# Kernel tuning notes

Hardware: AMD Instinct MI355X
Metric: run time of the kernel (lower is better)

## Reference

```python
import jax, jax.numpy as jnp
import numpy as np

NUM_HEADS = 4

def setup_inputs() -> dict:
    key = jax.random.key(0)
    ks = jax.random.split(key, 5)
    B, T, F, C = 2, 128, 256, 256
    # weights scaled ~1/sqrt(C) so softmax is not saturated
    s = 1.0 / np.sqrt(C)
    return {
        "x": jax.random.normal(ks[0], (B, T, F, C), jnp.float32),
        "w_in": jax.random.normal(ks[1], (3 * C, C), jnp.float32) * s,
        "b_in": jax.random.normal(ks[2], (3 * C,), jnp.float32) * 0.01,
        "w_out": jax.random.normal(ks[3], (C, C), jnp.float32) * s,
        "b_out": jax.random.normal(ks[4], (C,), jnp.float32) * 0.01,
        "band": 16,
    }

def reference(x, w_in, b_in, w_out, b_out, band):
    B, T, F, C = x.shape
    H = NUM_HEADS
    D = C // H
    x2 = x.reshape(B * T, F, C)  # attention over frequency, independent per (B,T)
    qkv = x2 @ w_in.T + b_in  # [BT, F, 3C]
    q, k, v = jnp.split(qkv, 3, axis=-1)
    def heads(t):
        return t.reshape(B * T, F, H, D).transpose(0, 2, 1, 3)  # [BT, H, F, D]
    q, k, v = heads(q), heads(k), heads(v)
    scores = jnp.einsum('bhid,bhjd->bhij', q, k) / jnp.sqrt(jnp.asarray(D, x.dtype))
    i = jnp.arange(F)[:, None]
    j = jnp.arange(F)[None, :]
    keep = jnp.abs(i - j) <= band  # banded locality mask [F, F]
    scores = jnp.where(keep, scores, -jnp.inf)
    attn = jax.nn.softmax(scores, axis=-1)
    out = jnp.einsum('bhij,bhjd->bhid', attn, v)  # [BT, H, F, D]
    out = out.transpose(0, 2, 1, 3).reshape(B * T, F, C)
    y = out @ w_out.T + b_out
    return y.reshape(B, T, F, C)
```

## Files before the change

### kernel.cpp

```cpp
#include <hip/hip_runtime.h>
#include <hip/hip_bf16.h>
#include <cstdint>

typedef unsigned int u32;
typedef __attribute__((ext_vector_type(8))) __bf16 bf16x8;
typedef __attribute__((ext_vector_type(4))) float f32x4;
typedef __attribute__((ext_vector_type(4))) _Float16 half4;
typedef __attribute__((ext_vector_type(2))) __fp16 fp16x2;

#define BT_N 256
#define F_N 256
#define C_N 256
#define H_N 4
#define D_N 64
#define TC_N 768
#define M_N (BT_N * F_N)
#define VT_ST 268

__device__ __forceinline__ ushort f2bf(float f) {
  u32 u = __float_as_uint(f);
  u32 r = (u + 0x7fffu + ((u >> 16) & 1u)) >> 16;
  return (ushort)r;
}

__device__ __forceinline__ u32 pkbf(float a, float b) {
  return (u32)f2bf(a) | ((u32)f2bf(b) << 16);
}

__device__ __forceinline__ void gload_lds16(const ushort* g, ushort* l) {
  __builtin_amdgcn_global_load_lds(
      (const __attribute__((address_space(1))) u32*)g,
      (__attribute__((address_space(3))) u32*)l, 16, 0, 0);
}

__global__ __launch_bounds__(256) void cvt3_f32_bf16_k(
    const float* __restrict__ sx, ushort* __restrict__ dx, int nx4,
    const float* __restrict__ si, ushort* __restrict__ di, int ni4,
    const float* __restrict__ so, ushort* __restrict__ dq, int no4) {
  int idx = blockIdx.x * 256 + threadIdx.x;
  int stride = gridDim.x * 256;
  int ntot = nx4 + ni4 + no4;
  for (int i = idx; i < ntot; i += stride) {
    const float4* s;
    ushort* d;
    if (i < nx4) { s = (const float4*)sx + i; d = dx + (size_t)i * 4; }
    else if (i < nx4 + ni4) { int k = i - nx4; s = (const float4*)si + k; d = di + (size_t)k * 4; }
    else { int k = i - nx4 - ni4; s = (const float4*)so + k; d = dq + (size_t)k * 4; }
    float4 v = *s;
    *(uint2*)d = make_uint2(pkbf(v.x, v.y), pkbf(v.z, v.w));
  }
}

__global__ __launch_bounds__(256, 4) void gemm_qkv_sb(
    const ushort* __restrict__ Ap, const ushort* __restrict__ Bp,
    const float* __restrict__ bias, _Float16* __restrict__ Cp,
    int NTN, int nwg8) {
  __shared__ ushort smemH[128 * 64 * 2];

  const int tid = threadIdx.x;
  const int lane = tid & 63;
  const int wid = tid >> 6;
  const int wr = wid >> 1, wc = wid & 1;
  const int l15 = lane & 15, l4 = lane >> 4;
  const int b = blockIdx.x;
  const int bid = (b & 7) * nwg8 + (b >> 3);
  const int tm = bid / NTN;
  const int tn = bid - tm * NTN;
  const int rowBase = tm * 128, colBase = tn * 128;

  f32x4 acc[4][4] = {};

  const int ar = (tid >> 3);
  const int c8 = tid & 7;
  const int akk = ((c8 ^ (ar & 7)) << 3);
  const ushort* gB = Bp + (size_t)(colBase + ar) * 256 + akk;
  const ushort* gAh = Ap + (size_t)(rowBase + ar) * 256 + akk;

#pragma unroll
  for (int t = 0; t < 4; ++t) {
    const int k0 = t * 64;
#pragma unroll
    for (int c = 0; c < 4; ++c) {
      gload_lds16(gAh + (size_t)(c * 32) * 256 + k0,
                  smemH + (size_t)(c * 256 + (wid << 6)) * 8);
      gload_lds16(gB + (size_t)(c * 32) * 256 + k0,
                  smemH + 8192 + (size_t)(c * 256 + (wid << 6)) * 8);
    }
    __syncthreads();
    const ushort* As_ = smemH;
    const ushort* Bs_ = smemH + 8192;
#pragma unroll
    for (int kk = 0; kk < 2; ++kk) {
      bf16x8 af[4];
      bf16x8 bfr[4];
#pragma unroll
      for (int i2 = 0; i2 < 4; ++i2) {
        int row = wr * 64 + i2 * 16 + l15;
        af[i2] = *(const bf16x8*)(As_ + row * 64 + (((kk * 4 + l4) ^ (l15 & 7)) * 8));
      }
#pragma unroll
      for (int j2 = 0; j2 < 4; ++j2) {
        int row = wc * 64 + j2 * 16 + l15;
        bfr[j2] = *(const bf16x8*)(Bs_ + row * 64 + (((kk * 4 + l4) ^ (l15 & 7)) * 8));
      }
#pragma unroll
      for (int i2 = 0; i2 < 4; ++i2)
#pragma unroll
        for (int j2 = 0; j2 < 4; ++j2)
          acc[i2][j2] = __builtin_amdgcn_mfma_f32_16x16x32_bf16(
              af[i2], bfr[j2], acc[i2][j2], 0, 0, 0);
    }
    __syncthreads();
  }

  ushort* eb = smemH;
#pragma unroll
  for (int pass = 0; pass < 2; ++pass) {
#pragma unroll
    for (int jh = 0; jh < 2; ++jh) {
      const int i2 = pass * 2 + jh;
#pragma unroll
      for (int j2 = 0; j2 < 4; ++j2) {
        float bv = bias[colBase + wc * 64 + j2 * 16 + l15];
#pragma unroll
        for (int r = 0; r < 4; ++r) {
          _Float16 h = (_Float16)(acc[i2][j2][r] + bv);
          eb[(wr * 32 + jh * 16 + l4 * 4 + r) * 136 + wc * 64 + j2 * 16 + l15] =
              __builtin_bit_cast(ushort, h);
        }
      }
    }
    __syncthreads();
#pragma unroll
    for (int i = 0; i < 8; ++i) {
      int br = wid * 16 + 2 * i + (lane >> 5);
      int hl = lane & 31;
      uint2 d = *(const uint2*)(eb + br * 136 + hl * 4);
      int grow = rowBase + (br >> 5) * 64 + pass * 32 + (br & 31);
      *(uint2*)(Cp + (size_t)grow * TC_N + colBase + hl * 4) = d;
    }
    __syncthreads();
  }
}

__global__ __launch_bounds__(256, 4) void gemm_out_sb(
    const ushort* __restrict__ Ap, const ushort* __restrict__ Bp,
    const float* __restrict__ bias, float* __restrict__ Cp,
    int NTN, int nwg8) {
  __shared__ char smem[64 * 132 * 4];
  ushort* smemH = (ushort*)smem;

  const int tid = threadIdx.x;
  const int lane = tid & 63;
  const int wid = tid >> 6;
  const int wr = wid >> 1, wc = wid & 1;
  const int l15 = lane & 15, l4 = lane >> 4;
  const int b = blockIdx.x;
  const int bid = (b & 7) * nwg8 + (b >> 3);
  const int tm = bid / NTN;
  const int tn = bid - tm * NTN;
  const int rowBase = tm * 128, colBase = tn * 128;

  f32x4 acc[4][4] = {};

  const int ar = (tid >> 3);
  const int c8 = tid & 7;
  const int akk = ((c8 ^ (ar & 7)) << 3);
  const ushort* gB = Bp + (size_t)(colBase + ar) * 256 + akk;
  const ushort* gAh = Ap + (size_t)(rowBase + ar) * 256 + akk;

#pragma unroll
  for (int t = 0; t < 4; ++t) {
    const int k0 = t * 64;
#pragma unroll
    for (int c = 0; c < 4; ++c) {
      gload_lds16(gAh + (size_t)(c * 32) * 256 + k0,
                  smemH + (size_t)(c * 256 + (wid << 6)) * 8);
      gload_lds16(gB + (size_t)(c * 32) * 256 + k0,
                  smemH + 8192 + (size_t)(c * 256 + (wid << 6)) * 8);
    }
    __syncthreads();
    const ushort* As_ = smemH;
    const ushort* Bs_ = smemH + 8192;
#pragma unroll
    for (int kk = 0; kk < 2; ++kk) {
      bf16x8 af[4];
      bf16x8 bfr[4];
#pragma unroll
      for (int i2 = 0; i2 < 4; ++i2) {
        int row = wr * 64 + i2 * 16 + l15;
        af[i2] = *(const bf16x8*)(As_ + row * 64 + (((kk * 4 + l4) ^ (l15 & 7)) * 8));
      }
#pragma unroll
      for (int j2 = 0; j2 < 4; ++j2) {
        int row = wc * 64 + j2 * 16 + l15;
        bfr[j2] = *(const bf16x8*)(Bs_ + row * 64 + (((kk * 4 + l4) ^ (l15 & 7)) * 8));
      }
#pragma unroll
      for (int i2 = 0; i2 < 4; ++i2)
#pragma unroll
        for (int j2 = 0; j2 < 4; ++j2)
          acc[i2][j2] = __builtin_amdgcn_mfma_f32_16x16x32_bf16(
              af[i2], bfr[j2], acc[i2][j2], 0, 0, 0);
    }
    __syncthreads();
  }

  float* eb = (float*)smem;
#pragma unroll
  for (int pass = 0; pass < 2; ++pass) {
#pragma unroll
    for (int jh = 0; jh < 2; ++jh) {
      const int i2 = pass * 2 + jh;
#pragma unroll
      for (int j2 = 0; j2 < 4; ++j2) {
        float bv = bias[colBase + wc * 64 + j2 * 16 + l15];
#pragma unroll
        for (int r = 0; r < 4; ++r)
          eb[(wr * 32 + jh * 16 + l4 * 4 + r) * 132 + wc * 64 + j2 * 16 + l15] =
              acc[i2][j2][r] + bv;
      }
    }
    __syncthreads();
#pragma unroll
    for (int i = 0; i < 16; ++i) {
      int br = wid * 16 + i;
      uint2 d = *(const uint2*)((const u32*)eb + br * 132 + lane * 2);
      int grow = rowBase + (br >> 5) * 64 + pass * 32 + (br & 31);
      *(uint2*)(Cp + (size_t)grow * C_N + colBase + lane * 2) = d;
    }
    __syncthreads();
  }
}

__global__ __launch_bounds__(256) void attn_mfma(
    const _Float16* __restrict__ qkv, ushort* __restrict__ aout) {
  __shared__ ushort smem[18432 + 64 * VT_ST];
  const int tid = threadIdx.x;
  const int bt = blockIdx.x >> 2;
  const int h = blockIdx.x & 3;
  const _Float16* base = qkv + (size_t)bt * 256 * 768 + h * 64;
  ushort* klds = smem;
  ushort* vlds = smem + 18432;

  {
    const int r0 = tid >> 3, c8 = tid & 7;
    const int pr2 = tid >> 4, dq = tid & 15;
#pragma unroll
    for (int p = 0; p < 8; ++p) {
      int j = p * 32 + r0;
      const uint4 k4 = *(const uint4*)(base + (size_t)j * 768 + 256 + c8 * 8);
      *(uint4*)(klds + j * 72 + c8 * 8) = k4;
      int j0 = p * 32 + pr2 * 2;
      uint2 va = *(const uint2*)(base + (size_t)j0 * 768 + 512 + dq * 4);
      uint2 vb = *(const uint2*)(base + (size_t)(j0 + 1) * 768 + 512 + dq * 4);
      u32 w0 = (va.x & 0xffffu) | (vb.x << 16);
      u32 w1 = (va.x >> 16) | (vb.x & 0xffff0000u);
      u32 w2 = (va.y & 0xffffu) | (vb.y << 16);
      u32 w3 = (va.y >> 16) | (vb.y & 0xffff0000u);
      int d0 = dq * 4;
      *(u32*)(vlds + (d0 + 0) * VT_ST + j0) = w0;
      *(u32*)(vlds + (d0 + 1) * VT_ST + j0) = w1;
      *(u32*)(vlds + (d0 + 2) * VT_ST + j0) = w2;
      *(u32*)(vlds + (d0 + 3) * VT_ST + j0) = w3;
    }
  }

  const int w = tid >> 6, lane = tid & 63;
  const int l15 = lane & 15, g = lane >> 4, g4 = g * 4;

  uint2 qf0[4], qf1[4], qf2[4], qf3[4];
  {
    const uint2* q0 = (const uint2*)(base + (size_t)(w * 64 + 0 * 16 + l15) * 768 + g4);
    const uint2* q1 = (const uint2*)(base + (size_t)(w * 64 + 1 * 16 + l15) * 768 + g4);
    const uint2* q2 = (const uint2*)(base + (size_t)(w * 64 + 2 * 16 + l15) * 768 + g4);
    const uint2* q3 = (const uint2*)(base + (size_t)(w * 64 + 3 * 16 + l15) * 768 + g4);
#pragma unroll
    for (int ks = 0; ks < 4; ++ks) {
      qf0[ks] = q0[ks * 4]; qf1[ks] = q1[ks * 4];
      qf2[ks] = q2[ks * 4]; qf3[ks] = q3[ks * 4];
    }
  }

  u32 bb = 0;
#pragma unroll
  for (int jt = 0; jt < 3; ++jt)
#pragma unroll
    for (int r = 0; r < 4; ++r) {
      int d = 16 * jt + g4 + r - 16 - l15;
      if (d >= -16 && d <= 16) bb |= 1u << (jt * 4 + r);
    }

  __syncthreads();

  const float SC = 0.18033688f;

#pragma unroll
  for (int rt = 0; rt < 4; ++rt) {
    const int R0 = w * 64 + rt * 16;
    const int Jc = R0 - 16;
    const uint2* qf = (rt == 0) ? qf0 : (rt == 1) ? qf1 : (rt == 2) ? qf2 : qf3;

    f32x4 st[3] = {};
#pragma unroll
    for (int jt = 0; jt < 3; ++jt) {
      int krow = Jc + 16 * jt + l15;
      krow = krow < 0 ? 0 : (krow > 255 ? 255 : krow);
      const ushort* kp = klds + krow * 72 + g4;
#pragma unroll
      for (int ks = 0; ks < 4; ++ks) {
        uint2 kf = *(const uint2*)(kp + ks * 16);
        st[jt] = __builtin_amdgcn_mfma_f32_16x16x16f16(
            __builtin_bit_cast(half4, kf), __builtin_bit_cast(half4, qf[ks]),
            st[jt], 0, 0, 0);
      }
    }

    float l_acc = 0.f;
    float pp[3][4];
#pragma unroll
    for (int jt = 0; jt < 3; ++jt)
#pragma unroll
      for (int r = 0; r < 4; ++r) {
        int jg = Jc + 16 * jt + g4 + r;
        bool keep = (((bb >> (jt * 4 + r)) & 1u) != 0) && (jg >= 0) && (jg < 256);
        float pv = keep ? __builtin_amdgcn_exp2f(st[jt][r] * SC) : 0.f;
        pp[jt][r] = pv;
        l_acc += pv;
      }
    l_acc += __shfl_xor(l_acc, 16, 64);
    l_acc += __shfl_xor(l_acc, 32, 64);
    const float inv = 1.f / l_acc;

    uint2 pf[3];
#pragma unroll
    for (int jt = 0; jt < 3; ++jt) {
      fp16x2 a = __builtin_amdgcn_cvt_pkrtz(pp[jt][0] * inv, pp[jt][1] * inv);
      fp16x2 c = __builtin_amdgcn_cvt_pkrtz(pp[jt][2] * inv, pp[jt][3] * inv);
      pf[jt].x = __builtin_bit_cast(u32, a);
      pf[jt].y = __builtin_bit_cast(u32, c);
    }

    f32x4 ot[4] = {};
#pragma unroll
    for (int kt = 0; kt < 3; ++kt) {
      int jb = Jc + 16 * kt + g4;
      jb = jb < 0 ? 0 : (jb > 252 ? 252 : jb);
#pragma unroll
      for (int mt = 0; mt < 4; ++mt) {
        uint2 vfr = *(const uint2*)(vlds + (16 * mt + l15) * VT_ST + jb);
        ot[mt] = __builtin_amdgcn_mfma_f32_16x16x16f16(
            __builtin_bit_cast(half4, vfr), __builtin_bit_cast(half4, pf[kt]),
            ot[mt], 0, 0, 0);
      }
    }

    ushort* orow = aout + (size_t)(bt * 256 + R0 + l15) * 256 + h * 64 + g4;
#pragma unroll
    for (int mt = 0; mt < 4; ++mt) {
      u32 lo = (u32)f2bf(ot[mt][0]) | ((u32)f2bf(ot[mt][1]) << 16);
      u32 hi = (u32)f2bf(ot[mt][2]) | ((u32)f2bf(ot[mt][3]) << 16);
      *(uint2*)(orow + mt * 16) = make_uint2(lo, hi);
    }
  }
}

extern "C" void kernel_launch(void* const* d_in, const int* in_sizes, int n_in,
                              void* d_out, int out_size, void* d_ws, size_t ws_size,
                              hipStream_t stream) {
  const float* x = (const float*)d_in[0];
  const float* w_in = (const float*)d_in[1];
  const float* b_in = (const float*)d_in[2];
  const float* w_out = (const float*)d_in[3];
  const float* b_out = (const float*)d_in[4];
  float* y = (float*)d_out;

  char* ws = (char*)d_ws;
  const size_t qkv_bytes = (size_t)M_N * TC_N * 2;
  const size_t xb_bytes = (size_t)M_N * C_N * 2;
  _Float16* qkv = (_Float16*)ws;
  ushort* xb = (ushort*)(ws + qkv_bytes);
  ushort* attn = xb;
  ushort* winb = (ushort*)(ws + qkv_bytes + xb_bytes);
  ushort* woutb = winb + TC_N * C_N;

  cvt3_f32_bf16_k<<<2048, 256, 0, stream>>>(x, xb, M_N * C_N / 4,
                                            w_in, winb, TC_N * C_N / 4,
                                            w_out, woutb, C_N * C_N / 4);

  gemm_qkv_sb<<<(M_N / 128) * (TC_N / 128), 256, 0, stream>>>(
      xb, winb, b_in, qkv, TC_N / 128, (M_N / 128) * (TC_N / 128) / 8);

  attn_mfma<<<BT_N * H_N, 256, 0, stream>>>(qkv, attn);

  gemm_out_sb<<<(M_N / 128) * (C_N / 128), 256, 0, stream>>>(
      attn, woutb, b_out, y, C_N / 128, (M_N / 128) * (C_N / 128) / 8);
}
```

Before: 99.28 us.

## Fuse x fp32-to-bf16 conversion into QKV GEMM A-tile loads

Stops converting the whole x tensor to bf16 in a separate pass. The QKV GEMM now loads fp32 x tiles straight into LDS with a swizzled layout and converts them to bf16 when building the MFMA fragments. This removes the write and re-read of a 32MB bf16 copy of x. In exchange the GEMM reads twice the A bytes, each x tile is re-read and re-converted by all six column-tile workgroups, LDS use grows to 48KB, and occupancy drops to 3 workgroups.

```diff
diff --git a/kernel.cpp b/kernel.cpp
--- a/kernel.cpp
+++ b/kernel.cpp
@@ -32,30 +32,32 @@
       (const __attribute__((address_space(1))) u32*)g,
       (__attribute__((address_space(3))) u32*)l, 16, 0, 0);
 }
-
-__global__ __launch_bounds__(256) void cvt3_f32_bf16_k(
-    const float* __restrict__ sx, ushort* __restrict__ dx, int nx4,
-    const float* __restrict__ si, ushort* __restrict__ di, int ni4,
-    const float* __restrict__ so, ushort* __restrict__ dq, int no4) {
+__device__ __forceinline__ void gload_lds16f(const float* g, float* l) {
+  __builtin_amdgcn_global_load_lds(
+      (const __attribute__((address_space(1))) u32*)g,
+      (__attribute__((address_space(3))) u32*)l, 16, 0, 0);
+}
+
+__global__ __launch_bounds__(256) void cvt2_f32_bf16_k(
+    const float* __restrict__ s0, ushort* __restrict__ d0, int n0,
+    const float* __restrict__ s1, ushort* __restrict__ d1, int n1) {
   int idx = blockIdx.x * 256 + threadIdx.x;
   int stride = gridDim.x * 256;
-  int ntot = nx4 + ni4 + no4;
-  for (int i = idx; i < ntot; i += stride) {
-    const float4* s;
-    ushort* d;
-    if (i < nx4) { s = (const float4*)sx + i; d = dx + (size_t)i * 4; }
-    else if (i < nx4 + ni4) { int k = i - nx4; s = (const float4*)si + k; d = di + (size_t)k * 4; }
-    else { int k = i - nx4 - ni4; s = (const float4*)so + k; d = dq + (size_t)k * 4; }
+  for (int i = idx; i < n0 + n1; i += stride) {
+    const float4* s = (i < n0) ? ((const float4*)s0 + i) : ((const float4*)s1 + (i - n0));
+    ushort* d = (i < n0) ? (d0 + (size_t)i * 4) : (d1 + (size_t)(i - n0) * 4);
     float4 v = *s;
     *(uint2*)d = make_uint2(pkbf(v.x, v.y), pkbf(v.z, v.w));
   }
 }
 
-__global__ __launch_bounds__(256, 4) void gemm_qkv_sb(
-    const ushort* __restrict__ Ap, const ushort* __restrict__ Bp,
+__global__ __launch_bounds__(256, 3) void gemm_qkv_f32(
+    const float* __restrict__ x, const ushort* __restrict__ Bp,
     const float* __restrict__ bias, _Float16* __restrict__ Cp,
     int NTN, int nwg8) {
-  __shared__ ushort smemH[128 * 64 * 2];
+  __shared__ char smem[49152];
+  float* Af = (float*)smem;
+  ushort* Bs = (ushort*)(smem + 32768);
 
   const int tid = threadIdx.x;
   const int lane = tid & 63;
@@ -70,25 +72,29 @@
 
   f32x4 acc[4][4] = {};
 
-  const int ar = (tid >> 3);
+  const int lr = lane >> 4;
+  const int ld = lane & 15;
+  const int r7a = (wid * 4 + lr) & 7;
+  const int csrc = (((ld >> 1) ^ r7a) * 2 + (ld & 1)) * 4;
+  const float* gA = x + (size_t)(rowBase + wid * 4 + lr) * 256 + csrc;
+
+  const int ar = tid >> 3;
   const int c8 = tid & 7;
   const int akk = ((c8 ^ (ar & 7)) << 3);
   const ushort* gB = Bp + (size_t)(colBase + ar) * 256 + akk;
-  const ushort* gAh = Ap + (size_t)(rowBase + ar) * 256 + akk;
 
 #pragma unroll
   for (int t = 0; t < 4; ++t) {
     const int k0 = t * 64;
 #pragma unroll
-    for (int c = 0; c < 4; ++c) {
-      gload_lds16(gAh + (size_t)(c * 32) * 256 + k0,
-                  smemH + (size_t)(c * 256 + (wid << 6)) * 8);
+    for (int p = 0; p < 8; ++p)
+      gload_lds16f(gA + (size_t)(p * 16) * 256 + k0,
+                   Af + (p * 16 + wid * 4) * 64);
+#pragma unroll
+    for (int c = 0; c < 4; ++c)
       gload_lds16(gB + (size_t)(c * 32) * 256 + k0,
-                  smemH + 8192 + (size_t)(c * 256 + (wid << 6)) * 8);
-    }
-    __syncthreads();
-    const ushort* As_ = smemH;
-    const ushort* Bs_ = smemH + 8192;
+                  Bs + (size_t)(c * 256 + (wid << 6)) * 8);
+    __syncthreads();
 #pragma unroll
     for (int kk = 0; kk < 2; ++kk) {
       bf16x8 af[4];
@@ -96,12 +102,18 @@
 #pragma unroll
       for (int i2 = 0; i2 < 4; ++i2) {
         int row = wr * 64 + i2 * 16 + l15;
-        af[i2] = *(const bf16x8*)(As_ + row * 64 + (((kk * 4 + l4) ^ (l15 & 7)) * 8));
+        int pair = (kk * 4 + l4) ^ (row & 7);
+        const float* fp = Af + row * 64 + pair * 8;
+        float4 fa = *(const float4*)fp;
+        float4 fb = *(const float4*)(fp + 4);
+        uint4 pk = make_uint4(pkbf(fa.x, fa.y), pkbf(fa.z, fa.w),
+                              pkbf(fb.x, fb.y), pkbf(fb.z, fb.w));
+        af[i2] = __builtin_bit_cast(bf16x8, pk);
       }
 #pragma unroll
       for (int j2 = 0; j2 < 4; ++j2) {
         int row = wc * 64 + j2 * 16 + l15;
-        bfr[j2] = *(const bf16x8*)(Bs_ + row * 64 + (((kk * 4 + l4) ^ (l15 & 7)) * 8));
+        bfr[j2] = *(const bf16x8*)(Bs + row * 64 + (((kk * 4 + l4) ^ (l15 & 7)) * 8));
       }
 #pragma unroll
       for (int i2 = 0; i2 < 4; ++i2)
@@ -113,7 +125,7 @@
     __syncthreads();
   }
 
-  ushort* eb = smemH;
+  ushort* eb = (ushort*)smem;
 #pragma unroll
   for (int pass = 0; pass < 2; ++pass) {
 #pragma unroll
@@ -377,19 +389,16 @@
 
   char* ws = (char*)d_ws;
   const size_t qkv_bytes = (size_t)M_N * TC_N * 2;
-  const size_t xb_bytes = (size_t)M_N * C_N * 2;
   _Float16* qkv = (_Float16*)ws;
-  ushort* xb = (ushort*)(ws + qkv_bytes);
-  ushort* attn = xb;
-  ushort* winb = (ushort*)(ws + qkv_bytes + xb_bytes);
+  ushort* attn = (ushort*)(ws + qkv_bytes);
+  ushort* winb = attn + (size_t)M_N * C_N;
   ushort* woutb = winb + TC_N * C_N;
 
-  cvt3_f32_bf16_k<<<2048, 256, 0, stream>>>(x, xb, M_N * C_N / 4,
-                                            w_in, winb, TC_N * C_N / 4,
-                                            w_out, woutb, C_N * C_N / 4);
-
-  gemm_qkv_sb<<<(M_N / 128) * (TC_N / 128), 256, 0, stream>>>(
-      xb, winb, b_in, qkv, TC_N / 128, (M_N / 128) * (TC_N / 128) / 8);
+  cvt2_f32_bf16_k<<<256, 256, 0, stream>>>(w_in, winb, TC_N * C_N / 4,
+                                           w_out, woutb, C_N * C_N / 4);
+
+  gemm_qkv_f32<<<(M_N / 128) * (TC_N / 128), 256, 0, stream>>>(
+      x, winb, b_in, qkv, TC_N / 128, (M_N / 128) * (TC_N / 128) / 8);
 
   attn_mfma<<<BT_N * H_N, 256, 0, stream>>>(qkv, attn);
 
```

After: 108.0 us. +8.8%, slower.
